# Optimization experiments

Hardware: AMD Instinct MI355X
Metric: run time of the kernel (lower is better)

## Reference

```python
import jax, jax.numpy as jnp
import numpy as np

N = 10000
IN_DIM = 1024
HID = 128
LAT = 64
E = 320000


def setup_inputs() -> dict:
    key = jax.random.key(0)
    ks = jax.random.split(key, 12)
    def glorot(k, shape):
        lim = float(np.sqrt(6.0 / (shape[0] + shape[1])))
        return jax.random.uniform(k, shape, jnp.float32, -lim, lim)
    x = jax.random.normal(ks[0], (N, IN_DIM), jnp.float32)
    edge_index = jax.random.randint(ks[1], (2, E), 0, N, jnp.int64)
    return {
        "x": x,
        "edge_index": edge_index,
        "W_enc1": glorot(ks[2], (IN_DIM, HID)), "b_enc1": jnp.zeros((HID,), jnp.float32),
        "W_enc2": glorot(ks[3], (HID, LAT)),   "b_enc2": jnp.zeros((LAT,), jnp.float32),
        "W_att1": glorot(ks[4], (LAT, HID)),   "b_att1": jnp.zeros((HID,), jnp.float32),
        "W_att2": glorot(ks[5], (HID, IN_DIM)),"b_att2": jnp.zeros((IN_DIM,), jnp.float32),
        "W_str":  glorot(ks[6], (LAT, LAT)),   "b_str":  jnp.zeros((LAT,), jnp.float32),
    }


def _gcn_norm(edge_index, n):
    # PyG GCNConv default: add self-loops, symmetric normalization
    loop = jnp.arange(n, dtype=edge_index.dtype)
    send = jnp.concatenate([edge_index[0], loop])
    recv = jnp.concatenate([edge_index[1], loop])
    deg = jax.ops.segment_sum(jnp.ones_like(recv, dtype=jnp.float32), recv, num_segments=n)
    dis = jnp.where(deg > 0, jax.lax.rsqrt(deg), 0.0)
    norm = dis[send] * dis[recv]  # [E+N]
    return send, recv, norm


def _gcn(x, W, b, send, recv, norm, n):
    h = x @ W                                  # [N, out]
    msg = h[send] * norm[:, None]              # gather + scale
    agg = jax.ops.segment_sum(msg, recv, num_segments=n)  # scatter-add
    return agg + b


def reference(x, edge_index, W_enc1, b_enc1, W_enc2, b_enc2,
              W_att1, b_att1, W_att2, b_att2, W_str, b_str):
    n = x.shape[0]
    send, recv, norm = _gcn_norm(edge_index, n)
    # encoder
    h = jax.nn.relu(_gcn(x, W_enc1, b_enc1, send, recv, norm, n))
    z = jax.nn.relu(_gcn(h, W_enc2, b_enc2, send, recv, norm, n))
    # attribute decoder
    a = jax.nn.relu(_gcn(z, W_att1, b_att1, send, recv, norm, n))
    attr_recon = jax.nn.relu(_gcn(a, W_att2, b_att2, send, recv, norm, n))
    # structure decoder
    s = jax.nn.relu(_gcn(z, W_str, b_str, send, recv, norm, n))
    struct_recon = s @ s.T  # [N, N]
    return (attr_recon, struct_recon, z)
```

## Files before the change

### kernel.cpp

```cpp
#include <hip/hip_runtime.h>
#include <hip/hip_bf16.h>

#define IN_DIM 1024
#define HID 128
#define LAT 64
#define DEGPAD 128

typedef __attribute__((ext_vector_type(8))) short bf16x8;
typedef __attribute__((ext_vector_type(4))) short bf16x4;
typedef __attribute__((ext_vector_type(4))) float f32x4;


__global__ __launch_bounds__(256) void k_initcur(int* cursor, int n) {
    int i = blockIdx.x * 256 + threadIdx.x;
    if (i < n) cursor[i] = 0;
}

__global__ __launch_bounds__(256) void k_fillpad(const int* __restrict__ ei, int* cursor,
                                                 int* __restrict__ colPad, int E) {
    int e = blockIdx.x * 256 + threadIdx.x;
    if (e >= E) return;
    int s = ei[e], r = ei[E + e];
    int slot = atomicAdd(&cursor[r], 1);
    if (slot < DEGPAD) colPad[(size_t)r * DEGPAD + slot] = s;
}

__global__ __launch_bounds__(256) void k_dis(const int* __restrict__ cursor, float* dis, int n) {
    int i = blockIdx.x * 256 + threadIdx.x;
    if (i < n) dis[i] = rsqrtf((float)(cursor[i] + 1));
}


#define W1T_OFF 0
#define W2T_OFF 131072
#define Wa1T_OFF 139264
#define Wa2T_OFF 147456
#define WsT_OFF 278528
#define WT_TOTAL 282624

__global__ __launch_bounds__(256) void k_wsplit(const float* __restrict__ W1, const float* __restrict__ W2,
                                                const float* __restrict__ Wa1, const float* __restrict__ Wa2,
                                                const float* __restrict__ Ws,
                                                __hip_bfloat16* __restrict__ hi, __hip_bfloat16* __restrict__ lo) {
    int idx = blockIdx.x * 256 + threadIdx.x;
    if (idx >= WT_TOTAL) return;
    const float* src; int base, shK, Nc;
    if (idx < W2T_OFF)       { src = W1;  base = W1T_OFF;  shK = 10; Nc = 128; }
    else if (idx < Wa1T_OFF) { src = W2;  base = W2T_OFF;  shK = 7;  Nc = 64; }
    else if (idx < Wa2T_OFF) { src = Wa1; base = Wa1T_OFF; shK = 6;  Nc = 128; }
    else if (idx < WsT_OFF)  { src = Wa2; base = Wa2T_OFF; shK = 7;  Nc = 1024; }
    else                     { src = Ws;  base = WsT_OFF;  shK = 6;  Nc = 64; }
    int local = idx - base;
    int nn = local >> shK;
    int k = local & ((1 << shK) - 1);
    float v = src[(size_t)k * Nc + nn];
    __hip_bfloat16 h = __float2bfloat16(v);
    hi[idx] = h;
    lo[idx] = __float2bfloat16(v - __bfloat162float(h));
}


template<int F, bool BIAS, bool RELU, int OMODE>
__global__ __launch_bounds__(256) void k_spmm(const float* __restrict__ Hin,
                                              const int* __restrict__ colPad,
                                              const int* __restrict__ cursor,
                                              const float* __restrict__ dis,
                                              const float* __restrict__ bias,
                                              float* __restrict__ out, float* __restrict__ out2,
                                              __hip_bfloat16* __restrict__ ohi,
                                              __hip_bfloat16* __restrict__ olo, int n) {
    int wave = (blockIdx.x * 256 + threadIdx.x) >> 6;
    int lane = threadIdx.x & 63;
    if (wave >= n) return;
    int d = cursor[wave];
    if (d > DEGPAD) d = DEGPAD;
    const int* cp = colPad + (size_t)wave * DEGPAD;
    float acc[F / 64];
    const float* self = Hin + (size_t)wave * F;
#pragma unroll
    for (int j = 0; j < F / 64; ++j) acc[j] = self[lane + 64 * j];
    for (int p = 0; p < d; ++p) {
        int c = cp[p];
        const float* row = Hin + (size_t)c * F;
#pragma unroll
        for (int j = 0; j < F / 64; ++j) acc[j] += row[lane + 64 * j];
    }
    float di = dis[wave];
#pragma unroll
    for (int j = 0; j < F / 64; ++j) {
        float r = acc[j] * di;
        if (BIAS) r += bias[lane + 64 * j];
        if (RELU) r = fmaxf(r, 0.f);
        size_t idx = (size_t)wave * F + lane + 64 * j;
        if constexpr (OMODE == 1) {
            __hip_bfloat16 h = __float2bfloat16(r);
            ohi[idx] = h;
            olo[idx] = __float2bfloat16(r - __bfloat162float(h));
        } else {
            out[idx] = r;
            if constexpr (OMODE == 2) out2[idx] = r * di;
        }
    }
}


template<int AMODE, bool BIAS, bool RELU, bool DIS, bool SPLITOUT, bool NT>
__global__ __launch_bounds__(256) void k_gemm_mfma(
        const __hip_bfloat16* __restrict__ Ahi, const __hip_bfloat16* __restrict__ Alo,
        const float* __restrict__ Af,
        const __hip_bfloat16* __restrict__ Bthi, const __hip_bfloat16* __restrict__ Btlo,
        const float* __restrict__ bias, const float* __restrict__ dis,
        float* __restrict__ Cf, __hip_bfloat16* __restrict__ Chi, __hip_bfloat16* __restrict__ Clo,
        int M, int K, int Nc) {
    __shared__ float tile[128 * 68];
    int tid = threadIdx.x;
    int w = tid >> 6, lane = tid & 63;
    int wr = w >> 1, wc = w & 1;
    int m0 = blockIdx.y * 128, n0 = blockIdx.x * 64;
    int lrow = lane & 15, lk = (lane >> 4) * 8;

    int arow[4];
    size_t aoff[4];
#pragma unroll
    for (int mi = 0; mi < 4; ++mi) {
        arow[mi] = m0 + wr * 64 + mi * 16 + lrow;
        aoff[mi] = (size_t)arow[mi] * K + lk;
    }
    size_t boff[2];
#pragma unroll
    for (int nj = 0; nj < 2; ++nj)
        boff[nj] = (size_t)(n0 + wc * 32 + nj * 16 + lrow) * K + lk;

    f32x4 acc[4][2] = {};

    for (int k0 = 0; k0 < K; k0 += 32) {
        bf16x8 bh[2], bl[2], ah[4], al[4];
#pragma unroll
        for (int nj = 0; nj < 2; ++nj) {
            bh[nj] = *(const bf16x8*)(Bthi + boff[nj] + k0);
            bl[nj] = *(const bf16x8*)(Btlo + boff[nj] + k0);
        }
        if constexpr (AMODE == 0) {
#pragma unroll
            for (int mi = 0; mi < 4; ++mi) {
                ah[mi] = *(const bf16x8*)(Ahi + aoff[mi] + k0);
                al[mi] = *(const bf16x8*)(Alo + aoff[mi] + k0);
            }
        } else {
#pragma unroll
            for (int mi = 0; mi < 4; ++mi) {
                float4 f0 = make_float4(0.f, 0.f, 0.f, 0.f), f1 = f0;
                if (arow[mi] < M) {
                    f0 = *(const float4*)(Af + aoff[mi] + k0);
                    f1 = *(const float4*)(Af + aoff[mi] + k0 + 4);
                }
                float ff[8] = {f0.x, f0.y, f0.z, f0.w, f1.x, f1.y, f1.z, f1.w};
                __attribute__((aligned(16))) __hip_bfloat16 hb[8], lb[8];
#pragma unroll
                for (int t = 0; t < 8; ++t) {
                    __hip_bfloat16 h = __float2bfloat16(ff[t]);
                    hb[t] = h;
                    lb[t] = __float2bfloat16(ff[t] - __bfloat162float(h));
                }
                ah[mi] = *(const bf16x8*)hb;
                al[mi] = *(const bf16x8*)lb;
            }
        }
#pragma unroll
        for (int mi = 0; mi < 4; ++mi)
#pragma unroll
            for (int nj = 0; nj < 2; ++nj) {
                acc[mi][nj] = __builtin_amdgcn_mfma_f32_16x16x32_bf16(ah[mi], bh[nj], acc[mi][nj], 0, 0, 0);
                acc[mi][nj] = __builtin_amdgcn_mfma_f32_16x16x32_bf16(ah[mi], bl[nj], acc[mi][nj], 0, 0, 0);
                acc[mi][nj] = __builtin_amdgcn_mfma_f32_16x16x32_bf16(al[mi], bh[nj], acc[mi][nj], 0, 0, 0);
            }
    }

    int r0 = (lane >> 4) * 4;
#pragma unroll
    for (int mi = 0; mi < 4; ++mi)
#pragma unroll
        for (int nj = 0; nj < 2; ++nj) {
            int cl = wc * 32 + nj * 16 + lrow;
#pragma unroll
            for (int r = 0; r < 4; ++r) {
                int rl = wr * 64 + mi * 16 + r0 + r;
                tile[rl * 68 + cl] = acc[mi][nj][r];
            }
        }
    __syncthreads();

#pragma unroll
    for (int it = 0; it < 8; ++it) {
        int rl = it * 16 + (tid >> 4);
        int c4 = tid & 15;
        int row = m0 + rl;
        if (row >= M) continue;
        int col = n0 + c4 * 4;
        float4 v = *(const float4*)&tile[rl * 68 + c4 * 4];
        if (BIAS) {
            float4 b = *(const float4*)&bias[col];
            v.x += b.x; v.y += b.y; v.z += b.z; v.w += b.w;
        }
        if (RELU) {
            v.x = fmaxf(v.x, 0.f); v.y = fmaxf(v.y, 0.f);
            v.z = fmaxf(v.z, 0.f); v.w = fmaxf(v.w, 0.f);
        }
        if (DIS) {
            float di = dis[row];
            v.x *= di; v.y *= di; v.z *= di; v.w *= di;
        }
        if constexpr (SPLITOUT) {
            float vv[4] = {v.x, v.y, v.z, v.w};
            __attribute__((aligned(8))) __hip_bfloat16 hs[4], ls[4];
#pragma unroll
            for (int k = 0; k < 4; ++k) {
                hs[k] = __float2bfloat16(vv[k]);
                ls[k] = __float2bfloat16(vv[k] - __bfloat162float(hs[k]));
            }
            *(bf16x4*)&Chi[(size_t)row * Nc + col] = *(bf16x4*)hs;
            *(bf16x4*)&Clo[(size_t)row * Nc + col] = *(bf16x4*)ls;
        } else if constexpr (NT) {
            __builtin_nontemporal_store(*(const f32x4*)&v, (f32x4*)&Cf[(size_t)row * Nc + col]);
        } else {
            *(float4*)&Cf[(size_t)row * Nc + col] = v;
        }
    }
}


__device__ __forceinline__ int swz(int rl, int c4) { return (c4 ^ (rl & 31)); }

__global__ __launch_bounds__(256) void k_sst_mfma(const __hip_bfloat16* __restrict__ Shi,
                                                  const __hip_bfloat16* __restrict__ Slo,
                                                  float* __restrict__ C, int M) {
    int bx = blockIdx.x, by = blockIdx.y;
    if (by < bx) return;
    __shared__ float tile[128 * 128];

    int w = threadIdx.x >> 6, lane = threadIdx.x & 63;
    int wr = w >> 1, wc = w & 1;
    int i0 = bx * 128 + wr * 64;
    int j0 = by * 128 + wc * 64;
    int lrow = lane & 15;
    int lk = (lane >> 4) * 8;

    f32x4 acc[4][4] = {};

#pragma unroll
    for (int ks = 0; ks < 2; ++ks) {
        bf16x8 ah[4], al[4], bh[4], bl[4];
#pragma unroll
        for (int mi = 0; mi < 4; ++mi) {
            size_t off = (size_t)(i0 + mi * 16 + lrow) * 64 + ks * 32 + lk;
            ah[mi] = *(const bf16x8*)(Shi + off);
            al[mi] = *(const bf16x8*)(Slo + off);
        }
#pragma unroll
        for (int nj = 0; nj < 4; ++nj) {
            size_t off = (size_t)(j0 + nj * 16 + lrow) * 64 + ks * 32 + lk;
            bh[nj] = *(const bf16x8*)(Shi + off);
            bl[nj] = *(const bf16x8*)(Slo + off);
        }
#pragma unroll
        for (int mi = 0; mi < 4; ++mi)
#pragma unroll
            for (int nj = 0; nj < 4; ++nj) {
                acc[mi][nj] = __builtin_amdgcn_mfma_f32_16x16x32_bf16(ah[mi], bh[nj], acc[mi][nj], 0, 0, 0);
                acc[mi][nj] = __builtin_amdgcn_mfma_f32_16x16x32_bf16(ah[mi], bl[nj], acc[mi][nj], 0, 0, 0);
                acc[mi][nj] = __builtin_amdgcn_mfma_f32_16x16x32_bf16(al[mi], bh[nj], acc[mi][nj], 0, 0, 0);
            }
    }

    int r0 = (lane >> 4) * 4;
#pragma unroll
    for (int mi = 0; mi < 4; ++mi)
#pragma unroll
        for (int nj = 0; nj < 4; ++nj) {
#pragma unroll
            for (int r = 0; r < 4; ++r) {
                int rl = wr * 64 + mi * 16 + r0 + r;
                int cl = wc * 64 + nj * 16 + lrow;
                tile[rl * 128 + (swz(rl, cl >> 2) << 2) + (cl & 3)] = acc[mi][nj][r];
            }
        }
    __syncthreads();

    int i0b = bx * 128, j0b = by * 128;
    int tt = threadIdx.x;

#pragma unroll
    for (int it = 0; it < 16; ++it) {
        int rl = it * 8 + (tt >> 5);
        int c4 = tt & 31;
        int row = i0b + rl;
        if (row >= M) continue;
        int col = j0b + c4 * 4;
        if (col >= M) continue;
        float4 v = *(const float4*)&tile[rl * 128 + (swz(rl, c4) << 2)];
        if (col + 3 < M) {
            __builtin_nontemporal_store(*(const f32x4*)&v, (f32x4*)&C[(size_t)row * M + col]);
        } else {
            float vv[4] = {v.x, v.y, v.z, v.w};
            for (int k = 0; k < 4 && col + k < M; ++k) C[(size_t)row * M + col + k] = vv[k];
        }
    }

    if (bx != by) {
#pragma unroll
        for (int it = 0; it < 16; ++it) {
            int cl = it * 8 + (tt >> 5);
            int row = j0b + cl;
            if (row >= M) continue;
            int rbase = (tt & 31) * 4;
            int col = i0b + rbase;
            if (col >= M) continue;
            float vv[4];
#pragma unroll
            for (int k = 0; k < 4; ++k) {
                int rr = rbase + k;
                vv[k] = tile[rr * 128 + (swz(rr, cl >> 2) << 2) + (cl & 3)];
            }
            if (col + 3 < M) {
                float4 v = make_float4(vv[0], vv[1], vv[2], vv[3]);
                __builtin_nontemporal_store(*(const f32x4*)&v, (f32x4*)&C[(size_t)row * M + col]);
            } else {
                for (int k = 0; k < 4 && col + k < M; ++k) C[(size_t)row * M + col + k] = vv[k];
            }
        }
    }
}


extern "C" void kernel_launch(void* const* d_in, const int* in_sizes, int n_in,
                              void* d_out, int out_size, void* d_ws, size_t ws_size,
                              hipStream_t stream) {
    const float* x   = (const float*)d_in[0];
    const int*   ei  = (const int*)d_in[1];
    const float* W1  = (const float*)d_in[2];
    const float* b1  = (const float*)d_in[3];
    const float* W2  = (const float*)d_in[4];
    const float* b2  = (const float*)d_in[5];
    const float* Wa1 = (const float*)d_in[6];
    const float* ba1 = (const float*)d_in[7];
    const float* Wa2 = (const float*)d_in[8];
    const float* ba2 = (const float*)d_in[9];
    const float* Ws  = (const float*)d_in[10];
    const float* bs  = (const float*)d_in[11];

    int N = in_sizes[0] / IN_DIM;
    int E = in_sizes[1] / 2;
    int Mpad = ((N + 127) / 128) * 128;

    float* out  = (float*)d_out;
    float* attr = out;
    float* st   = out + (size_t)N * IN_DIM;
    float* zout = st + (size_t)N * N;

    char* basep = (char*)d_ws;
    size_t off = 0;
    auto alloc = [&](size_t bytes) -> void* {
        void* p = basep + off;
        off = (off + bytes + 255) & ~(size_t)255;
        return p;
    };

    int*   colPad = (int*)alloc((size_t)N * DEGPAD * 4);
    int*   cursor = (int*)alloc((size_t)N * 4);
    float* dis    = (float*)alloc((size_t)N * 4);
    __hip_bfloat16* Whi = (__hip_bfloat16*)alloc((size_t)WT_TOTAL * 2);
    __hip_bfloat16* Wlo = (__hip_bfloat16*)alloc((size_t)WT_TOTAL * 2);
    float* t128 = (float*)alloc((size_t)N * 128 * 4);
    float* t64  = (float*)alloc((size_t)N * 64 * 4);
    float* zp   = (float*)alloc((size_t)N * 64 * 4);
    __hip_bfloat16* Hhi  = (__hip_bfloat16*)alloc((size_t)Mpad * 128 * 2);
    __hip_bfloat16* Hlo  = (__hip_bfloat16*)alloc((size_t)Mpad * 128 * 2);
    __hip_bfloat16* AZhi = (__hip_bfloat16*)alloc((size_t)Mpad * 64 * 2);
    __hip_bfloat16* AZlo = (__hip_bfloat16*)alloc((size_t)Mpad * 64 * 2);
    __hip_bfloat16* AAhi = (__hip_bfloat16*)alloc((size_t)Mpad * 128 * 2);
    __hip_bfloat16* AAlo = (__hip_bfloat16*)alloc((size_t)Mpad * 128 * 2);
    __hip_bfloat16* Shi  = (__hip_bfloat16*)alloc((size_t)Mpad * 64 * 2);
    __hip_bfloat16* Slo  = (__hip_bfloat16*)alloc((size_t)Mpad * 64 * 2);

    dim3 b256(256);
    int nb_n = (N + 255) / 256;
    int spmm_grid = (N * 64 + 255) / 256;

    k_initcur<<<dim3(nb_n), b256, 0, stream>>>(cursor, N);
    k_wsplit<<<dim3((WT_TOTAL + 255) / 256), b256, 0, stream>>>(W1, W2, Wa1, Wa2, Ws, Whi, Wlo);
    k_fillpad<<<dim3((E + 255) / 256), b256, 0, stream>>>(ei, cursor, colPad, E);
    k_dis<<<dim3(nb_n), b256, 0, stream>>>(cursor, dis, N);

    k_gemm_mfma<1, false, false, true, false, false><<<dim3(2, Mpad / 128), b256, 0, stream>>>(
        nullptr, nullptr, x, Whi + W1T_OFF, Wlo + W1T_OFF, nullptr, dis,
        t128, nullptr, nullptr, N, 1024, 128);
    k_spmm<128, true, true, 1><<<dim3(spmm_grid), b256, 0, stream>>>(
        t128, colPad, cursor, dis, b1, nullptr, nullptr, Hhi, Hlo, N);
    k_gemm_mfma<0, false, false, true, false, false><<<dim3(1, Mpad / 128), b256, 0, stream>>>(
        Hhi, Hlo, nullptr, Whi + W2T_OFF, Wlo + W2T_OFF, nullptr, dis,
        t64, nullptr, nullptr, N, 128, 64);
    k_spmm<64, true, true, 2><<<dim3(spmm_grid), b256, 0, stream>>>(
        t64, colPad, cursor, dis, b2, zout, zp, nullptr, nullptr, N);
    k_spmm<64, false, false, 1><<<dim3(spmm_grid), b256, 0, stream>>>(
        zp, colPad, cursor, dis, nullptr, nullptr, nullptr, AZhi, AZlo, N);
    k_gemm_mfma<0, true, true, true, false, false><<<dim3(2, Mpad / 128), b256, 0, stream>>>(
        AZhi, AZlo, nullptr, Whi + Wa1T_OFF, Wlo + Wa1T_OFF, ba1, dis,
        t128, nullptr, nullptr, N, 64, 128);
    k_spmm<128, false, false, 1><<<dim3(spmm_grid), b256, 0, stream>>>(
        t128, colPad, cursor, dis, nullptr, nullptr, nullptr, AAhi, AAlo, N);
    k_gemm_mfma<0, true, true, false, false, true><<<dim3(16, Mpad / 128), b256, 0, stream>>>(
        AAhi, AAlo, nullptr, Whi + Wa2T_OFF, Wlo + Wa2T_OFF, ba2, nullptr,
        attr, nullptr, nullptr, N, 128, 1024);
    k_gemm_mfma<0, true, true, false, true, false><<<dim3(1, Mpad / 128), b256, 0, stream>>>(
        AZhi, AZlo, nullptr, Whi + WsT_OFF, Wlo + WsT_OFF, bs, nullptr,
        nullptr, Shi, Slo, N, 64, 64);
    k_sst_mfma<<<dim3(Mpad / 128, Mpad / 128), b256, 0, stream>>>(Shi, Slo, st, N);
}
```

Measured before the change: 367.8 us.

## Fuse GCN pipeline into fewer launches and fold normalization into SpMM

Merges the cursor reset and weight split into one prep kernel. Edge bucketing and the first x@W1 GEMM now share one kernel, the two small decoder GEMMs share another, and the attribute GEMM and the S·Sᵀ product share a final tail kernel, all through a shared device GEMM routine. The precomputed dis array and the pre-scaled zp buffer are gone; SpMM recomputes rsqrt(deg+1) for the node and for each neighbour from the cursor array. The intent is to cut launch count and intermediate traffic. In exchange, the structure product is now a generic 128x64 tiled GEMM that computes the full N×N output instead of using symmetry, and each SpMM neighbour costs an extra cursor gather.

```diff
diff --git a/kernel.cpp b/kernel.cpp
--- a/kernel.cpp
+++ b/kernel.cpp
@@ -9,27 +9,6 @@
 typedef __attribute__((ext_vector_type(8))) short bf16x8;
 typedef __attribute__((ext_vector_type(4))) short bf16x4;
 typedef __attribute__((ext_vector_type(4))) float f32x4;
-
-
-__global__ __launch_bounds__(256) void k_initcur(int* cursor, int n) {
-    int i = blockIdx.x * 256 + threadIdx.x;
-    if (i < n) cursor[i] = 0;
-}
-
-__global__ __launch_bounds__(256) void k_fillpad(const int* __restrict__ ei, int* cursor,
-                                                 int* __restrict__ colPad, int E) {
-    int e = blockIdx.x * 256 + threadIdx.x;
-    if (e >= E) return;
-    int s = ei[e], r = ei[E + e];
-    int slot = atomicAdd(&cursor[r], 1);
-    if (slot < DEGPAD) colPad[(size_t)r * DEGPAD + slot] = s;
-}
-
-__global__ __launch_bounds__(256) void k_dis(const int* __restrict__ cursor, float* dis, int n) {
-    int i = blockIdx.x * 256 + threadIdx.x;
-    if (i < n) dis[i] = rsqrtf((float)(cursor[i] + 1));
-}
-
 
 #define W1T_OFF 0
 #define W2T_OFF 131072
@@ -38,85 +17,24 @@
 #define WsT_OFF 278528
 #define WT_TOTAL 282624
 
-__global__ __launch_bounds__(256) void k_wsplit(const float* __restrict__ W1, const float* __restrict__ W2,
-                                                const float* __restrict__ Wa1, const float* __restrict__ Wa2,
-                                                const float* __restrict__ Ws,
-                                                __hip_bfloat16* __restrict__ hi, __hip_bfloat16* __restrict__ lo) {
-    int idx = blockIdx.x * 256 + threadIdx.x;
-    if (idx >= WT_TOTAL) return;
-    const float* src; int base, shK, Nc;
-    if (idx < W2T_OFF)       { src = W1;  base = W1T_OFF;  shK = 10; Nc = 128; }
-    else if (idx < Wa1T_OFF) { src = W2;  base = W2T_OFF;  shK = 7;  Nc = 64; }
-    else if (idx < Wa2T_OFF) { src = Wa1; base = Wa1T_OFF; shK = 6;  Nc = 128; }
-    else if (idx < WsT_OFF)  { src = Wa2; base = Wa2T_OFF; shK = 7;  Nc = 1024; }
-    else                     { src = Ws;  base = WsT_OFF;  shK = 6;  Nc = 64; }
-    int local = idx - base;
-    int nn = local >> shK;
-    int k = local & ((1 << shK) - 1);
-    float v = src[(size_t)k * Nc + nn];
-    __hip_bfloat16 h = __float2bfloat16(v);
-    hi[idx] = h;
-    lo[idx] = __float2bfloat16(v - __bfloat162float(h));
-}
-
-
-template<int F, bool BIAS, bool RELU, int OMODE>
-__global__ __launch_bounds__(256) void k_spmm(const float* __restrict__ Hin,
-                                              const int* __restrict__ colPad,
-                                              const int* __restrict__ cursor,
-                                              const float* __restrict__ dis,
-                                              const float* __restrict__ bias,
-                                              float* __restrict__ out, float* __restrict__ out2,
-                                              __hip_bfloat16* __restrict__ ohi,
-                                              __hip_bfloat16* __restrict__ olo, int n) {
-    int wave = (blockIdx.x * 256 + threadIdx.x) >> 6;
-    int lane = threadIdx.x & 63;
-    if (wave >= n) return;
-    int d = cursor[wave];
-    if (d > DEGPAD) d = DEGPAD;
-    const int* cp = colPad + (size_t)wave * DEGPAD;
-    float acc[F / 64];
-    const float* self = Hin + (size_t)wave * F;
-#pragma unroll
-    for (int j = 0; j < F / 64; ++j) acc[j] = self[lane + 64 * j];
-    for (int p = 0; p < d; ++p) {
-        int c = cp[p];
-        const float* row = Hin + (size_t)c * F;
-#pragma unroll
-        for (int j = 0; j < F / 64; ++j) acc[j] += row[lane + 64 * j];
-    }
-    float di = dis[wave];
-#pragma unroll
-    for (int j = 0; j < F / 64; ++j) {
-        float r = acc[j] * di;
-        if (BIAS) r += bias[lane + 64 * j];
-        if (RELU) r = fmaxf(r, 0.f);
-        size_t idx = (size_t)wave * F + lane + 64 * j;
-        if constexpr (OMODE == 1) {
-            __hip_bfloat16 h = __float2bfloat16(r);
-            ohi[idx] = h;
-            olo[idx] = __float2bfloat16(r - __bfloat162float(h));
-        } else {
-            out[idx] = r;
-            if constexpr (OMODE == 2) out2[idx] = r * di;
-        }
-    }
-}
-
-
-template<int AMODE, bool BIAS, bool RELU, bool DIS, bool SPLITOUT, bool NT>
-__global__ __launch_bounds__(256) void k_gemm_mfma(
+__device__ __forceinline__ void splitf(float v, __hip_bfloat16& h, __hip_bfloat16& l) {
+    h = __float2bfloat16(v);
+    l = __float2bfloat16(v - __bfloat162float(h));
+}
+
+
+template<int AMODE, bool BIAS, bool RELU, bool SPLITOUT, bool NT, bool CGUARD>
+__device__ void dev_gemm(float* smem, int bx, int byy,
         const __hip_bfloat16* __restrict__ Ahi, const __hip_bfloat16* __restrict__ Alo,
         const float* __restrict__ Af,
         const __hip_bfloat16* __restrict__ Bthi, const __hip_bfloat16* __restrict__ Btlo,
-        const float* __restrict__ bias, const float* __restrict__ dis,
+        const float* __restrict__ bias,
         float* __restrict__ Cf, __hip_bfloat16* __restrict__ Chi, __hip_bfloat16* __restrict__ Clo,
-        int M, int K, int Nc) {
-    __shared__ float tile[128 * 68];
+        int M, int K, int ldc, int ncol) {
     int tid = threadIdx.x;
     int w = tid >> 6, lane = tid & 63;
     int wr = w >> 1, wc = w & 1;
-    int m0 = blockIdx.y * 128, n0 = blockIdx.x * 64;
+    int m0 = byy * 128, n0 = bx * 64;
     int lrow = lane & 15, lk = (lane >> 4) * 8;
 
     int arow[4];
@@ -157,11 +75,7 @@
                 float ff[8] = {f0.x, f0.y, f0.z, f0.w, f1.x, f1.y, f1.z, f1.w};
                 __attribute__((aligned(16))) __hip_bfloat16 hb[8], lb[8];
 #pragma unroll
-                for (int t = 0; t < 8; ++t) {
-                    __hip_bfloat16 h = __float2bfloat16(ff[t]);
-                    hb[t] = h;
-                    lb[t] = __float2bfloat16(ff[t] - __bfloat162float(h));
-                }
+                for (int t = 0; t < 8; ++t) splitf(ff[t], hb[t], lb[t]);
                 ah[mi] = *(const bf16x8*)hb;
                 al[mi] = *(const bf16x8*)lb;
             }
@@ -185,7 +99,7 @@
 #pragma unroll
             for (int r = 0; r < 4; ++r) {
                 int rl = wr * 64 + mi * 16 + r0 + r;
-                tile[rl * 68 + cl] = acc[mi][nj][r];
+                smem[rl * 68 + cl] = acc[mi][nj][r];
             }
         }
     __syncthreads();
@@ -195,139 +109,177 @@
         int rl = it * 16 + (tid >> 4);
         int c4 = tid & 15;
         int row = m0 + rl;
-        if (row >= M) continue;
         int col = n0 + c4 * 4;
-        float4 v = *(const float4*)&tile[rl * 68 + c4 * 4];
-        if (BIAS) {
-            float4 b = *(const float4*)&bias[col];
-            v.x += b.x; v.y += b.y; v.z += b.z; v.w += b.w;
-        }
-        if (RELU) {
-            v.x = fmaxf(v.x, 0.f); v.y = fmaxf(v.y, 0.f);
-            v.z = fmaxf(v.z, 0.f); v.w = fmaxf(v.w, 0.f);
-        }
-        if (DIS) {
-            float di = dis[row];
-            v.x *= di; v.y *= di; v.z *= di; v.w *= di;
-        }
-        if constexpr (SPLITOUT) {
-            float vv[4] = {v.x, v.y, v.z, v.w};
-            __attribute__((aligned(8))) __hip_bfloat16 hs[4], ls[4];
-#pragma unroll
-            for (int k = 0; k < 4; ++k) {
-                hs[k] = __float2bfloat16(vv[k]);
-                ls[k] = __float2bfloat16(vv[k] - __bfloat162float(hs[k]));
-            }
-            *(bf16x4*)&Chi[(size_t)row * Nc + col] = *(bf16x4*)hs;
-            *(bf16x4*)&Clo[(size_t)row * Nc + col] = *(bf16x4*)ls;
-        } else if constexpr (NT) {
-            __builtin_nontemporal_store(*(const f32x4*)&v, (f32x4*)&Cf[(size_t)row * Nc + col]);
+        bool ok = (row < M) && (!CGUARD || col < ncol);
+        if (ok) {
+            float4 v = *(const float4*)&smem[rl * 68 + c4 * 4];
+            if (BIAS) {
+                float4 b = *(const float4*)&bias[col];
+                v.x += b.x; v.y += b.y; v.z += b.z; v.w += b.w;
+            }
+            if (RELU) {
+                v.x = fmaxf(v.x, 0.f); v.y = fmaxf(v.y, 0.f);
+                v.z = fmaxf(v.z, 0.f); v.w = fmaxf(v.w, 0.f);
+            }
+            if constexpr (SPLITOUT) {
+                float vv[4] = {v.x, v.y, v.z, v.w};
+                __attribute__((aligned(8))) __hip_bfloat16 hs[4], ls[4];
+#pragma unroll
+                for (int k = 0; k < 4; ++k) splitf(vv[k], hs[k], ls[k]);
+                *(bf16x4*)&Chi[(size_t)row * ldc + col] = *(bf16x4*)hs;
+                *(bf16x4*)&Clo[(size_t)row * ldc + col] = *(bf16x4*)ls;
+            } else if constexpr (NT) {
+                __builtin_nontemporal_store(*(const f32x4*)&v, (f32x4*)&Cf[(size_t)row * ldc + col]);
+            } else {
+                *(float4*)&Cf[(size_t)row * ldc + col] = v;
+            }
+        }
+    }
+    __syncthreads();
+}
+
+
+__global__ __launch_bounds__(256) void k_prep(const float* __restrict__ W1, const float* __restrict__ W2,
+                                              const float* __restrict__ Wa1, const float* __restrict__ Wa2,
+                                              const float* __restrict__ Ws,
+                                              __hip_bfloat16* __restrict__ hi, __hip_bfloat16* __restrict__ lo,
+                                              int* cursor, int N) {
+    int gtid = blockIdx.x * 256 + threadIdx.x;
+    int gsz = gridDim.x * 256;
+    for (int i = gtid; i < N; i += gsz) cursor[i] = 0;
+    for (int idx = gtid; idx < WT_TOTAL; idx += gsz) {
+        const float* src; int base, shK, Nc;
+        if (idx < W2T_OFF)       { src = W1;  base = W1T_OFF;  shK = 10; Nc = 128; }
+        else if (idx < Wa1T_OFF) { src = W2;  base = W2T_OFF;  shK = 7;  Nc = 64; }
+        else if (idx < Wa2T_OFF) { src = Wa1; base = Wa1T_OFF; shK = 6;  Nc = 128; }
+        else if (idx < WsT_OFF)  { src = Wa2; base = Wa2T_OFF; shK = 7;  Nc = 1024; }
+        else                     { src = Ws;  base = WsT_OFF;  shK = 6;  Nc = 64; }
+        int local = idx - base;
+        int nn = local >> shK;
+        int k = local & ((1 << shK) - 1);
+        splitf(src[(size_t)k * Nc + nn], hi[idx], lo[idx]);
+    }
+}
+
+__global__ __launch_bounds__(256) void k_build(const int* __restrict__ ei, int* cursor,
+                                               int* __restrict__ colPad, int E,
+                                               const float* __restrict__ x,
+                                               const __hip_bfloat16* __restrict__ Whi,
+                                               const __hip_bfloat16* __restrict__ Wlo,
+                                               float* __restrict__ t128, int M, int Mpad) {
+    __shared__ float smem[128 * 68];
+    int gtid = blockIdx.x * 256 + threadIdx.x;
+    int gsz = gridDim.x * 256;
+    for (int e = gtid; e < E; e += gsz) {
+        int s = ei[e], r = ei[E + e];
+        int slot = atomicAdd(&cursor[r], 1);
+        if (slot < DEGPAD) colPad[(size_t)r * DEGPAD + slot] = s;
+    }
+    int nt2 = (Mpad / 128) * 2;
+    for (int t = blockIdx.x; t < nt2; t += gridDim.x)
+        dev_gemm<1, false, false, false, false, false>(smem, t & 1, t >> 1,
+            nullptr, nullptr, x, Whi + W1T_OFF, Wlo + W1T_OFF, nullptr,
+            t128, nullptr, nullptr, M, 1024, 128, 0);
+}
+
+template<int F, bool BIAS, bool RELU, int OMODE>
+__global__ __launch_bounds__(256) void k_spmm(const float* __restrict__ Hin,
+                                              const int* __restrict__ colPad,
+                                              const int* __restrict__ cursor,
+                                              const float* __restrict__ bias,
+                                              float* __restrict__ out,
+                                              __hip_bfloat16* __restrict__ ohi,
+                                              __hip_bfloat16* __restrict__ olo, int n) {
+    int i = (blockIdx.x * 256 + threadIdx.x) >> 6;
+    int lane = threadIdx.x & 63;
+    if (i >= n) return;
+    int d = cursor[i];
+    float di = rsqrtf((float)(d + 1));
+    if (d > DEGPAD) d = DEGPAD;
+    const int* cp = colPad + (size_t)i * DEGPAD;
+    float acc[F / 64];
+    const float* self = Hin + (size_t)i * F;
+#pragma unroll
+    for (int j = 0; j < F / 64; ++j) acc[j] = di * self[lane + 64 * j];
+    for (int p = 0; p < d; ++p) {
+        int c = cp[p];
+        float dc = rsqrtf((float)(cursor[c] + 1));
+        const float* row = Hin + (size_t)c * F;
+#pragma unroll
+        for (int j = 0; j < F / 64; ++j) acc[j] = fmaf(dc, row[lane + 64 * j], acc[j]);
+    }
+#pragma unroll
+    for (int j = 0; j < F / 64; ++j) {
+        float r = acc[j] * di;
+        if (BIAS) r += bias[lane + 64 * j];
+        if (RELU) r = fmaxf(r, 0.f);
+        size_t idx = (size_t)i * F + lane + 64 * j;
+        if constexpr (OMODE == 1) {
+            __hip_bfloat16 h, l;
+            splitf(r, h, l);
+            ohi[idx] = h; olo[idx] = l;
         } else {
-            *(float4*)&Cf[(size_t)row * Nc + col] = v;
-        }
-    }
-}
-
-
-__device__ __forceinline__ int swz(int rl, int c4) { return (c4 ^ (rl & 31)); }
-
-__global__ __launch_bounds__(256) void k_sst_mfma(const __hip_bfloat16* __restrict__ Shi,
-                                                  const __hip_bfloat16* __restrict__ Slo,
-                                                  float* __restrict__ C, int M) {
-    int bx = blockIdx.x, by = blockIdx.y;
-    if (by < bx) return;
-    __shared__ float tile[128 * 128];
-
-    int w = threadIdx.x >> 6, lane = threadIdx.x & 63;
-    int wr = w >> 1, wc = w & 1;
-    int i0 = bx * 128 + wr * 64;
-    int j0 = by * 128 + wc * 64;
-    int lrow = lane & 15;
-    int lk = (lane >> 4) * 8;
-
-    f32x4 acc[4][4] = {};
-
-#pragma unroll
-    for (int ks = 0; ks < 2; ++ks) {
-        bf16x8 ah[4], al[4], bh[4], bl[4];
-#pragma unroll
-        for (int mi = 0; mi < 4; ++mi) {
-            size_t off = (size_t)(i0 + mi * 16 + lrow) * 64 + ks * 32 + lk;
-            ah[mi] = *(const bf16x8*)(Shi + off);
-            al[mi] = *(const bf16x8*)(Slo + off);
-        }
-#pragma unroll
-        for (int nj = 0; nj < 4; ++nj) {
-            size_t off = (size_t)(j0 + nj * 16 + lrow) * 64 + ks * 32 + lk;
-            bh[nj] = *(const bf16x8*)(Shi + off);
-            bl[nj] = *(const bf16x8*)(Slo + off);
-        }
-#pragma unroll
-        for (int mi = 0; mi < 4; ++mi)
-#pragma unroll
-            for (int nj = 0; nj < 4; ++nj) {
-                acc[mi][nj] = __builtin_amdgcn_mfma_f32_16x16x32_bf16(ah[mi], bh[nj], acc[mi][nj], 0, 0, 0);
-                acc[mi][nj] = __builtin_amdgcn_mfma_f32_16x16x32_bf16(ah[mi], bl[nj], acc[mi][nj], 0, 0, 0);
-                acc[mi][nj] = __builtin_amdgcn_mfma_f32_16x16x32_bf16(al[mi], bh[nj], acc[mi][nj], 0, 0, 0);
-            }
-    }
-
-    int r0 = (lane >> 4) * 4;
-#pragma unroll
-    for (int mi = 0; mi < 4; ++mi)
-#pragma unroll
-        for (int nj = 0; nj < 4; ++nj) {
-#pragma unroll
-            for (int r = 0; r < 4; ++r) {
-                int rl = wr * 64 + mi * 16 + r0 + r;
-                int cl = wc * 64 + nj * 16 + lrow;
-                tile[rl * 128 + (swz(rl, cl >> 2) << 2) + (cl & 3)] = acc[mi][nj][r];
-            }
-        }
-    __syncthreads();
-
-    int i0b = bx * 128, j0b = by * 128;
-    int tt = threadIdx.x;
-
-#pragma unroll
-    for (int it = 0; it < 16; ++it) {
-        int rl = it * 8 + (tt >> 5);
-        int c4 = tt & 31;
-        int row = i0b + rl;
-        if (row >= M) continue;
-        int col = j0b + c4 * 4;
-        if (col >= M) continue;
-        float4 v = *(const float4*)&tile[rl * 128 + (swz(rl, c4) << 2)];
-        if (col + 3 < M) {
-            __builtin_nontemporal_store(*(const f32x4*)&v, (f32x4*)&C[(size_t)row * M + col]);
-        } else {
-            float vv[4] = {v.x, v.y, v.z, v.w};
-            for (int k = 0; k < 4 && col + k < M; ++k) C[(size_t)row * M + col + k] = vv[k];
-        }
-    }
-
-    if (bx != by) {
-#pragma unroll
-        for (int it = 0; it < 16; ++it) {
-            int cl = it * 8 + (tt >> 5);
-            int row = j0b + cl;
-            if (row >= M) continue;
-            int rbase = (tt & 31) * 4;
-            int col = i0b + rbase;
-            if (col >= M) continue;
-            float vv[4];
-#pragma unroll
-            for (int k = 0; k < 4; ++k) {
-                int rr = rbase + k;
-                vv[k] = tile[rr * 128 + (swz(rr, cl >> 2) << 2) + (cl & 3)];
-            }
-            if (col + 3 < M) {
-                float4 v = make_float4(vv[0], vv[1], vv[2], vv[3]);
-                __builtin_nontemporal_store(*(const f32x4*)&v, (f32x4*)&C[(size_t)row * M + col]);
-            } else {
-                for (int k = 0; k < 4 && col + k < M; ++k) C[(size_t)row * M + col + k] = vv[k];
-            }
-        }
+            out[idx] = r;
+        }
+    }
+}
+
+__global__ __launch_bounds__(256) void k_g2(const __hip_bfloat16* __restrict__ Hhi,
+                                            const __hip_bfloat16* __restrict__ Hlo,
+                                            const __hip_bfloat16* __restrict__ Whi,
+                                            const __hip_bfloat16* __restrict__ Wlo,
+                                            float* __restrict__ t64, int M) {
+    __shared__ float smem[128 * 68];
+    dev_gemm<0, false, false, false, false, false>(smem, 0, blockIdx.x,
+        Hhi, Hlo, nullptr, Whi + W2T_OFF, Wlo + W2T_OFF, nullptr,
+        t64, nullptr, nullptr, M, 128, 64, 0);
+}
+
+__global__ __launch_bounds__(256) void k_g34(const __hip_bfloat16* __restrict__ AZhi,
+                                             const __hip_bfloat16* __restrict__ AZlo,
+                                             const __hip_bfloat16* __restrict__ Whi,
+                                             const __hip_bfloat16* __restrict__ Wlo,
+                                             const float* __restrict__ ba1, const float* __restrict__ bs,
+                                             float* __restrict__ t128,
+                                             __hip_bfloat16* __restrict__ Shi, __hip_bfloat16* __restrict__ Slo,
+                                             int M, int Mpad) {
+    __shared__ float smem[128 * 68];
+    int nt2 = (Mpad / 128) * 2;
+    int t = blockIdx.x;
+    if (t < nt2)
+        dev_gemm<0, true, true, false, false, false>(smem, t & 1, t >> 1,
+            AZhi, AZlo, nullptr, Whi + Wa1T_OFF, Wlo + Wa1T_OFF, ba1,
+            t128, nullptr, nullptr, M, 64, 128, 0);
+    else
+        dev_gemm<0, true, true, true, false, false>(smem, 0, t - nt2,
+            AZhi, AZlo, nullptr, Whi + WsT_OFF, Wlo + WsT_OFF, bs,
+            nullptr, Shi, Slo, M, 64, 64, 0);
+}
+
+__global__ __launch_bounds__(256) void k_tail(const __hip_bfloat16* __restrict__ AAhi,
+                                              const __hip_bfloat16* __restrict__ AAlo,
+                                              const __hip_bfloat16* __restrict__ Whi,
+                                              const __hip_bfloat16* __restrict__ Wlo,
+                                              const float* __restrict__ ba2,
+                                              const __hip_bfloat16* __restrict__ Shi,
+                                              const __hip_bfloat16* __restrict__ Slo,
+                                              float* __restrict__ attr, float* __restrict__ st,
+                                              int M, int Mpad) {
+    __shared__ float smem[128 * 68];
+    int nt = Mpad / 128;
+    int nG5 = 16 * nt;
+    int t = blockIdx.x;
+    if (t < nG5) {
+        dev_gemm<0, true, true, false, true, false>(smem, t & 15, t >> 4,
+            AAhi, AAlo, nullptr, Whi + Wa2T_OFF, Wlo + Wa2T_OFF, ba2,
+            attr, nullptr, nullptr, M, 128, 1024, 0);
+    } else {
+        int tt = t - nG5;
+        int nt2 = 2 * nt;
+        int bi = tt / nt2, bj = tt - bi * nt2;
+        dev_gemm<0, false, false, false, true, true>(smem, bj, bi,
+            Shi, Slo, nullptr, Shi, Slo, nullptr,
+            st, nullptr, nullptr, M, 64, M, M);
     }
 }
 
@@ -351,6 +303,7 @@
     int N = in_sizes[0] / IN_DIM;
     int E = in_sizes[1] / 2;
     int Mpad = ((N + 127) / 128) * 128;
+    int nt = Mpad / 128;
 
     float* out  = (float*)d_out;
     float* attr = out;
@@ -364,15 +317,12 @@
         off = (off + bytes + 255) & ~(size_t)255;
         return p;
     };
-
     int*   colPad = (int*)alloc((size_t)N * DEGPAD * 4);
     int*   cursor = (int*)alloc((size_t)N * 4);
-    float* dis    = (float*)alloc((size_t)N * 4);
     __hip_bfloat16* Whi = (__hip_bfloat16*)alloc((size_t)WT_TOTAL * 2);
     __hip_bfloat16* Wlo = (__hip_bfloat16*)alloc((size_t)WT_TOTAL * 2);
     float* t128 = (float*)alloc((size_t)N * 128 * 4);
     float* t64  = (float*)alloc((size_t)N * 64 * 4);
-    float* zp   = (float*)alloc((size_t)N * 64 * 4);
     __hip_bfloat16* Hhi  = (__hip_bfloat16*)alloc((size_t)Mpad * 128 * 2);
     __hip_bfloat16* Hlo  = (__hip_bfloat16*)alloc((size_t)Mpad * 128 * 2);
     __hip_bfloat16* AZhi = (__hip_bfloat16*)alloc((size_t)Mpad * 64 * 2);
@@ -383,36 +333,20 @@
     __hip_bfloat16* Slo  = (__hip_bfloat16*)alloc((size_t)Mpad * 64 * 2);
 
     dim3 b256(256);
-    int nb_n = (N + 255) / 256;
     int spmm_grid = (N * 64 + 255) / 256;
 
-    k_initcur<<<dim3(nb_n), b256, 0, stream>>>(cursor, N);
-    k_wsplit<<<dim3((WT_TOTAL + 255) / 256), b256, 0, stream>>>(W1, W2, Wa1, Wa2, Ws, Whi, Wlo);
-    k_fillpad<<<dim3((E + 255) / 256), b256, 0, stream>>>(ei, cursor, colPad, E);
-    k_dis<<<dim3(nb_n), b256, 0, stream>>>(cursor, dis, N);
-
-    k_gemm_mfma<1, false, false, true, false, false><<<dim3(2, Mpad / 128), b256, 0, stream>>>(
-        nullptr, nullptr, x, Whi + W1T_OFF, Wlo + W1T_OFF, nullptr, dis,
-        t128, nullptr, nullptr, N, 1024, 128);
+    k_prep<<<dim3(1104), b256, 0, stream>>>(W1, W2, Wa1, Wa2, Ws, Whi, Wlo, cursor, N);
+    k_build<<<dim3(1280), b256, 0, stream>>>(ei, cursor, colPad, E, x, Whi, Wlo, t128, N, Mpad);
     k_spmm<128, true, true, 1><<<dim3(spmm_grid), b256, 0, stream>>>(
-        t128, colPad, cursor, dis, b1, nullptr, nullptr, Hhi, Hlo, N);
-    k_gemm_mfma<0, false, false, true, false, false><<<dim3(1, Mpad / 128), b256, 0, stream>>>(
-        Hhi, Hlo, nullptr, Whi + W2T_OFF, Wlo + W2T_OFF, nullptr, dis,
-        t64, nullptr, nullptr, N, 128, 64);
-    k_spmm<64, true, true, 2><<<dim3(spmm_grid), b256, 0, stream>>>(
-        t64, colPad, cursor, dis, b2, zout, zp, nullptr, nullptr, N);
+        t128, colPad, cursor, b1, nullptr, Hhi, Hlo, N);
+    k_g2<<<dim3(nt), b256, 0, stream>>>(Hhi, Hlo, Whi, Wlo, t64, N);
+    k_spmm<64, true, true, 0><<<dim3(spmm_grid), b256, 0, stream>>>(
+        t64, colPad, cursor, b2, zout, nullptr, nullptr, N);
     k_spmm<64, false, false, 1><<<dim3(spmm_grid), b256, 0, stream>>>(
-        zp, colPad, cursor, dis, nullptr, nullptr, nullptr, AZhi, AZlo, N);
-    k_gemm_mfma<0, true, true, true, false, false><<<dim3(2, Mpad / 128), b256, 0, stream>>>(
-        AZhi, AZlo, nullptr, Whi + Wa1T_OFF, Wlo + Wa1T_OFF, ba1, dis,
-        t128, nullptr, nullptr, N, 64, 128);
+        zout, colPad, cursor, nullptr, nullptr, AZhi, AZlo, N);
+    k_g34<<<dim3(3 * nt), b256, 0, stream>>>(AZhi, AZlo, Whi, Wlo, ba1, bs, t128, Shi, Slo, N, Mpad);
     k_spmm<128, false, false, 1><<<dim3(spmm_grid), b256, 0, stream>>>(
-        t128, colPad, cursor, dis, nullptr, nullptr, nullptr, AAhi, AAlo, N);
-    k_gemm_mfma<0, true, true, false, false, true><<<dim3(16, Mpad / 128), b256, 0, stream>>>(
-        AAhi, AAlo, nullptr, Whi + Wa2T_OFF, Wlo + Wa2T_OFF, ba2, nullptr,
-        attr, nullptr, nullptr, N, 128, 1024);
-    k_gemm_mfma<0, true, true, false, true, false><<<dim3(1, Mpad / 128), b256, 0, stream>>>(
-        AZhi, AZlo, nullptr, Whi + WsT_OFF, Wlo + WsT_OFF, bs, nullptr,
-        nullptr, Shi, Slo, N, 64, 64);
-    k_sst_mfma<<<dim3(Mpad / 128, Mpad / 128), b256, 0, stream>>>(Shi, Slo, st, N);
-}
+        t128, colPad, cursor, nullptr, nullptr, AAhi, AAlo, N);
+    k_tail<<<dim3(16 * nt + nt * 2 * nt), b256, 0, stream>>>(
+        AAhi, AAlo, Whi, Wlo, ba2, Shi, Slo, attr, st, N, Mpad);
+}
```

New measurement: 399.2 us. 8.5% more time.
